# Optimization experiments

Measured on AMD Instinct MI355X. Metric: run time of the kernel, lower is better.

The kernel has to match this reference:

```python
import jax, jax.numpy as jnp
import numpy as np

SEQ_LEN, IN_DIM = 120, 132
UNITS = (64, 128, 64)
N_LABELS = 101


def _lstm(x, W, U, b):
    """Keras-style LSTM with activation='relu', recurrent_activation='sigmoid'.
    x: (B,T,D), W: (D,4u), U: (u,4u), b: (4u,). Gate order i,f,c,o.
    Returns full hidden sequence (B,T,u)."""
    u = U.shape[0]
    # precompute input projections for all timesteps (big GEMM outside scan)
    xz = jnp.einsum('btd,dz->btz', x, W) + b  # (B,T,4u)

    def step(carry, z_t):
        h, c = carry
        z = z_t + h @ U  # (B,4u)
        i, f, g, o = jnp.split(z, 4, axis=-1)
        i = jax.nn.sigmoid(i)
        f = jax.nn.sigmoid(f)
        o = jax.nn.sigmoid(o)
        c = f * c + i * jax.nn.relu(g)
        h = o * jax.nn.relu(c)
        return (h, c), h

    B = x.shape[0]
    h0 = jnp.zeros((B, u), x.dtype)
    (_, _), hs = jax.lax.scan(step, (h0, h0), jnp.swapaxes(xz, 0, 1))
    return jnp.swapaxes(hs, 0, 1)  # (B,T,u)


def setup_inputs() -> dict:
    key = jax.random.key(0)
    ks = jax.random.split(key, 16)
    s = 0.05
    d = {'x': jax.random.normal(ks[0], (1024, SEQ_LEN, IN_DIM), jnp.float32)}
    in_dims = (IN_DIM,) + UNITS[:-1]
    for l, (din, u) in enumerate(zip(in_dims, UNITS), start=1):
        d[f'W{l}'] = jax.random.normal(ks[3 * l - 2], (din, 4 * u), jnp.float32) * s
        d[f'U{l}'] = jax.random.normal(ks[3 * l - 1], (u, 4 * u), jnp.float32) * s
        d[f'b{l}'] = jnp.zeros((4 * u,), jnp.float32)
    dense_dims = [(UNITS[-1], 64), (64, 32), (32, N_LABELS)]
    for l, (din, dout) in enumerate(dense_dims, start=1):
        d[f'Wd{l}'] = jax.random.normal(ks[9 + l], (din, dout), jnp.float32) * s
        d[f'bd{l}'] = jnp.zeros((dout,), jnp.float32)
    return d


def reference(x, W1, U1, b1, W2, U2, b2, W3, U3, b3,
              Wd1, bd1, Wd2, bd2, Wd3, bd3):
    h = _lstm(x, W1, U1, b1)          # (B,T,64)
    h = _lstm(h, W2, U2, b2)          # (B,T,128)
    h = _lstm(h, W3, U3, b3)[:, -1]   # return_sequences=False -> (B,64)
    h = jax.nn.relu(h @ Wd1 + bd1)    # (B,64)
    h = jax.nn.relu(h @ Wd2 + bd2)    # (B,32)
    return jax.nn.softmax(h @ Wd3 + bd3, axis=-1)  # (B,101)
```

## Files before the change

### kernel.cpp

```cpp
#include <hip/hip_runtime.h>
#include <math.h>

#define T_STEPS 120
#define BATCH   1024
#define NBK     64

typedef __attribute__((ext_vector_type(8))) short bf16x8;
typedef __attribute__((ext_vector_type(4))) float f32x4;
typedef __attribute__((ext_vector_type(4))) unsigned short us4;
typedef unsigned short u16;

__device__ __forceinline__ unsigned split2(float f) {
    union { float f; unsigned u; } a; a.f = f;
    unsigned hi = a.u >> 16;
    union { float f; unsigned u; } h; h.u = a.u & 0xFFFF0000u;
    union { float f; unsigned u; } b; b.f = f - h.f;
    unsigned rr = b.u + 0x7FFFu + ((b.u >> 16) & 1);
    return (hi << 16) | (rr >> 16);
}

__device__ __forceinline__ short bf16rne(float f) {
    union { float f; unsigned u; } a; a.f = f;
    unsigned r = a.u + 0x7FFFu + ((a.u >> 16) & 1);
    return (short)(r >> 16);
}

__device__ __forceinline__ float fast_sigmoid(float x) {
    float e = __expf(-x);
    return __builtin_amdgcn_rcpf(1.f + e);
}

__device__ __forceinline__ void block_sync_lds() {
    asm volatile("s_waitcnt lgkmcnt(0)" ::: "memory");
    __builtin_amdgcn_sched_barrier(0);
    __builtin_amdgcn_s_barrier();
    __builtin_amdgcn_sched_barrier(0);
}

__global__ __launch_bounds__(256)
void xconv(const float* __restrict__ x, u16* __restrict__ xf)
{
    int tid  = blockIdx.x * 256 + threadIdx.x;
    int lane = tid & 63;
    int rest = tid >> 6;
    int kt   = rest % 5;
    int tbk  = rest / 5;
    int bk   = tbk & 63;
    int t    = tbk >> 6;
    int ln   = lane & 15, lq = lane >> 4;
    int b    = bk * 16 + ln;
    int k0   = kt * 32 + lq * 8;
    const float* src = &x[((size_t)b * T_STEPS + t) * 132];
    u16 out[8];
#pragma unroll
    for (int e = 0; e < 8; ++e) {
        int k = k0 + e;
        out[e] = (u16)bf16rne((k < 132) ? src[k] : 0.f);
    }
    us4 o0, o1;
    o0.x = out[0]; o0.y = out[1]; o0.z = out[2]; o0.w = out[3];
    o1.x = out[4]; o1.y = out[5]; o1.z = out[6]; o1.w = out[7];
    *reinterpret_cast<us4*>(&xf[(size_t)tid * 8])     = o0;
    *reinterpret_cast<us4*>(&xf[(size_t)tid * 8 + 4]) = o1;
}

template<int U, int NBT, int KTXI, int KTXO, bool LAST_ONLY>
__global__ __launch_bounds__(512, 1)
void lstm_comb(const u16* __restrict__ xf,
               const float* __restrict__ W, int KIN,
               const float* __restrict__ Uw, const float* __restrict__ bias,
               u16* __restrict__ hf, float* __restrict__ hlast)
{
    constexpr int NZ  = 4 * U;
    constexpr int KTH = U / 32;
    constexpr int KXP = KTXI * 32;
    constexpr int HPLANE = NBT * U;
    constexpr int UG  = U / 16;
    constexpr size_t XSTRIDE = (size_t)NBK * KTXI * 512;
    constexpr size_t OSTRIDE = (size_t)NBK * KTXO * 512;
    static_assert(UG * (NBT / 16) == 8, "8 waves");

    __shared__ u16 hsh[4 * HPLANE];
    __shared__ u16 Wl[KXP * NZ];

    const int tid  = threadIdx.x;
    const int lane = tid & 63;
    const int wid  = tid >> 6;
    const int ln   = lane & 15;
    const int lq   = lane >> 4;
    const int ug   = wid % UG;
    const int bh   = wid / UG;
    const int unit = ug * 16 + ln;
    const int bb   = bh * 16;
    const int b0   = blockIdx.x * NBT;
    const int bkw  = (b0 + bb) >> 4;

    for (int idx = tid; idx < KXP * NZ; idx += 512) {
        int k = idx / NZ, n = idx % NZ;
        float f = (k < KIN) ? W[(size_t)k * NZ + n] : 0.f;
        Wl[((k >> 3) * NZ + n) * 8 + (k & 7)] = (u16)bf16rne(f);
    }

    bf16x8 bwu[4][KTH];
#pragma unroll
    for (int p = 0; p < 4; ++p)
#pragma unroll
        for (int kt = 0; kt < KTH; ++kt)
#pragma unroll
            for (int e = 0; e < 8; ++e) {
                int k = kt * 32 + lq * 8 + e;
                bwu[p][kt][e] = bf16rne(Uw[(size_t)k * NZ + p * U + unit]);
            }
    float breg[4];
#pragma unroll
    for (int p = 0; p < 4; ++p) breg[p] = bias[p * U + unit];

    u16* hw0 = hsh + ((unit >> 3) * NBT + bb + lq * 4) * 8 + (unit & 7);
    u16* hw1 = hw0 + 2 * HPLANE;
    float creg[4];
#pragma unroll
    for (int r = 0; r < 4; ++r) {
        creg[r] = 0.f;
        hw0[r * 8] = 0;
        hw0[HPLANE + r * 8] = 0;
    }

    const u16* hrd[2][KTH];
#pragma unroll
    for (int b = 0; b < 2; ++b)
#pragma unroll
        for (int kt = 0; kt < KTH; ++kt)
            hrd[b][kt] = hsh + b * 2 * HPLANE + ((kt * 4 + lq) * NBT + bb + ln) * 8;

    const u16* wb = Wl + ((size_t)lq * NZ + unit) * 8;

    const u16* pxf = xf + ((size_t)bkw * KTXI) * 512 + lane * 8;
    bf16x8 xfh[KTXI];
#pragma unroll
    for (int kt = 0; kt < KTXI; ++kt)
        xfh[kt] = *reinterpret_cast<const bf16x8*>(pxf + kt * 512);

    u16* hfo = nullptr;
    if constexpr (!LAST_ONLY) {
        int kto = unit >> 5;
        int lqp = (unit >> 3) & 3;
        int ep  = unit & 7;
        hfo = hf + (((size_t)bkw * KTXO + kto) * 64 + lqp * 16 + lq * 4) * 8 + ep;
    }

    block_sync_lds();

#define CSTEP(CUR, OTH, tc)                                                     \
    {                                                                           \
        f32x4 acc[4] = {};                                                      \
        _Pragma("unroll")                                                       \
        for (int kt = 0; kt < KTH; ++kt) {                                      \
            bf16x8 ahh = *reinterpret_cast<const bf16x8*>(hrd[CUR][kt]);        \
            bf16x8 ahl = *reinterpret_cast<const bf16x8*>(hrd[CUR][kt] + HPLANE); \
            _Pragma("unroll")                                                   \
            for (int p = 0; p < 4; ++p) {                                       \
                acc[p] = __builtin_amdgcn_mfma_f32_16x16x32_bf16(ahh, bwu[p][kt], acc[p], 0, 0, 0); \
                acc[p] = __builtin_amdgcn_mfma_f32_16x16x32_bf16(ahl, bwu[p][kt], acc[p], 0, 0, 0); \
            }                                                                   \
        }                                                                       \
        _Pragma("unroll")                                                       \
        for (int kt = 0; kt < KTXI; ++kt)                                       \
        _Pragma("unroll")                                                       \
        for (int p = 0; p < 4; ++p) {                                           \
            bf16x8 wf = *reinterpret_cast<const bf16x8*>(wb + ((size_t)kt * 4 * NZ + p * U) * 8); \
            acc[p] = __builtin_amdgcn_mfma_f32_16x16x32_bf16(xfh[kt], wf, acc[p], 0, 0, 0); \
        }                                                                       \
        if ((tc) + 1 < T_STEPS) {                                               \
            pxf += XSTRIDE;                                                     \
            _Pragma("unroll")                                                   \
            for (int kt = 0; kt < KTXI; ++kt)                                   \
                xfh[kt] = *reinterpret_cast<const bf16x8*>(pxf + kt * 512);     \
        }                                                                       \
        _Pragma("unroll")                                                       \
        for (int r = 0; r < 4; ++r) {                                           \
            float si = fast_sigmoid(acc[0][r] + breg[0]);                       \
            float sf = fast_sigmoid(acc[1][r] + breg[1]);                       \
            float gg = fmaxf(acc[2][r] + breg[2], 0.f);                         \
            float so = fast_sigmoid(acc[3][r] + breg[3]);                       \
            float c  = sf * creg[r] + si * gg;                                  \
            creg[r] = c;                                                        \
            float h = so * fmaxf(c, 0.f);                                       \
            unsigned s = split2(h);                                             \
            u16* hw = (OTH) ? hw1 : hw0;                                        \
            hw[r * 8] = (u16)(s >> 16);                                         \
            hw[HPLANE + r * 8] = (u16)s;                                        \
            if constexpr (!LAST_ONLY) {                                         \
                hfo[(size_t)(tc) * OSTRIDE + r * 8] = (u16)(s >> 16);           \
            } else {                                                            \
                if ((tc) == T_STEPS - 1)                                        \
                    hlast[(size_t)(b0 + bb + lq * 4 + r) * U + unit] = h;       \
            }                                                                   \
        }                                                                       \
        block_sync_lds();                                                       \
    }

    for (int t = 0; t < T_STEPS; t += 2) {
        CSTEP(0, 1, t)
        CSTEP(1, 0, t + 1)
    }
#undef CSTEP
}

__global__ __launch_bounds__(256)
void dense_head(const float* __restrict__ h3,
                const float* __restrict__ Wd1, const float* __restrict__ bd1,
                const float* __restrict__ Wd2, const float* __restrict__ bd2,
                const float* __restrict__ Wd3, const float* __restrict__ bd3,
                float* __restrict__ out)
{
    __shared__ float s1[4][64];
    __shared__ float s2[4][32];
    const int w    = threadIdx.x >> 6;
    const int lane = threadIdx.x & 63;
    const int row  = blockIdx.x * 4 + w;

    float hval = h3[(size_t)row * 64 + lane];
    float a = bd1[lane];
#pragma unroll
    for (int k = 0; k < 64; ++k) {
        float hk = __shfl(hval, k, 64);
        a = fmaf(hk, Wd1[k * 64 + lane], a);
    }
    s1[w][lane] = fmaxf(a, 0.f);
    __syncthreads();

    if (lane < 32) {
        float a2 = bd2[lane];
#pragma unroll
        for (int k = 0; k < 64; ++k) a2 = fmaf(s1[w][k], Wd2[k * 32 + lane], a2);
        s2[w][lane] = fmaxf(a2, 0.f);
    }
    __syncthreads();

    float a0 = bd3[lane];
#pragma unroll
    for (int k = 0; k < 32; ++k) a0 = fmaf(s2[w][k], Wd3[k * 101 + lane], a0);
    float a1 = -INFINITY;
    if (lane < 37) {
        a1 = bd3[64 + lane];
#pragma unroll
        for (int k = 0; k < 32; ++k) a1 = fmaf(s2[w][k], Wd3[k * 101 + 64 + lane], a1);
    }

    float m = fmaxf(a0, a1);
#pragma unroll
    for (int off = 32; off > 0; off >>= 1) m = fmaxf(m, __shfl_xor(m, off, 64));
    float e0 = expf(a0 - m);
    float e1 = (lane < 37) ? expf(a1 - m) : 0.f;
    float s = e0 + e1;
#pragma unroll
    for (int off = 32; off > 0; off >>= 1) s += __shfl_xor(s, off, 64);

    out[(size_t)row * 101 + lane] = e0 / s;
    if (lane < 37) out[(size_t)row * 101 + 64 + lane] = e1 / s;
}

extern "C" void kernel_launch(void* const* d_in, const int* in_sizes, int n_in,
                              void* d_out, int out_size, void* d_ws, size_t ws_size,
                              hipStream_t stream) {
    const float* x   = (const float*)d_in[0];
    const float* W1  = (const float*)d_in[1];
    const float* U1  = (const float*)d_in[2];
    const float* b1  = (const float*)d_in[3];
    const float* W2  = (const float*)d_in[4];
    const float* U2  = (const float*)d_in[5];
    const float* b2  = (const float*)d_in[6];
    const float* W3  = (const float*)d_in[7];
    const float* U3  = (const float*)d_in[8];
    const float* b3  = (const float*)d_in[9];
    const float* Wd1 = (const float*)d_in[10];
    const float* bd1 = (const float*)d_in[11];
    const float* Wd2 = (const float*)d_in[12];
    const float* bd2 = (const float*)d_in[13];
    const float* Wd3 = (const float*)d_in[14];
    const float* bd3 = (const float*)d_in[15];

    u16* ws16 = (u16*)d_ws;
    u16* xfb  = ws16;
    u16* h1f  = ws16 + 19660800;
    u16* h2f  = h1f + 7864320;
    float* h3 = (float*)(ws16 + 43253760);

    xconv<<<(T_STEPS * NBK * 5 * 64) / 256, 256, 0, stream>>>(x, xfb);
    lstm_comb<64, 32, 5, 2, false><<<32, 512, 0, stream>>>(
        xfb, W1, 132, U1, b1, h1f, nullptr);
    lstm_comb<128, 16, 2, 4, false><<<64, 512, 0, stream>>>(
        h1f, W2, 64, U2, b2, h2f, nullptr);
    lstm_comb<64, 32, 4, 1, true><<<32, 512, 0, stream>>>(
        h2f, W3, 128, U3, b3, nullptr, h3);
    dense_head<<<BATCH / 4, 256, 0, stream>>>(h3, Wd1, bd1, Wd2, bd2, Wd3, bd3,
                                              (float*)d_out);
}
```

Measured before the change: 495.8 us.

## Halve LSTM waves per block, give each wave two tiles, drop split-bf16 hidden state

Each LSTM block now runs 4 waves instead of 8, and each wave computes two 16x16 tiles, either two unit groups or two batch halves. Layers 1 and 3 hold their input weights in registers rather than LDS. The recurrent hidden state is stored as a single bf16 instead of a hi/lo bf16 pair, which halves the recurrent MFMAs and the LDS traffic. This is meant to cut barrier cost and per-step latency on the serial recurrence. The trade-off is lower precision in the recurrent matmul and more work per wave.

After: 601.3 us. 1.21x slower.

```diff
diff --git a/kernel.cpp b/kernel.cpp
--- a/kernel.cpp
+++ b/kernel.cpp
@@ -9,15 +9,6 @@
 typedef __attribute__((ext_vector_type(4))) float f32x4;
 typedef __attribute__((ext_vector_type(4))) unsigned short us4;
 typedef unsigned short u16;
-
-__device__ __forceinline__ unsigned split2(float f) {
-    union { float f; unsigned u; } a; a.f = f;
-    unsigned hi = a.u >> 16;
-    union { float f; unsigned u; } h; h.u = a.u & 0xFFFF0000u;
-    union { float f; unsigned u; } b; b.f = f - h.f;
-    unsigned rr = b.u + 0x7FFFu + ((b.u >> 16) & 1);
-    return (hi << 16) | (rr >> 16);
-}
 
 __device__ __forceinline__ short bf16rne(float f) {
     union { float f; unsigned u; } a; a.f = f;
@@ -64,146 +55,210 @@
     *reinterpret_cast<us4*>(&xf[(size_t)tid * 8 + 4]) = o1;
 }
 
-template<int U, int NBT, int KTXI, int KTXO, bool LAST_ONLY>
-__global__ __launch_bounds__(512, 1)
-void lstm_comb(const u16* __restrict__ xf,
-               const float* __restrict__ W, int KIN,
-               const float* __restrict__ Uw, const float* __restrict__ bias,
-               u16* __restrict__ hf, float* __restrict__ hlast)
+template<int U, int NBT, int KTXI, int KTXO, bool UNITPH, bool WXLDS, bool LAST_ONLY>
+__global__ __launch_bounds__(256, 1)
+__attribute__((amdgpu_waves_per_eu(1, 1)))
+void lstm_ph(const u16* __restrict__ xf,
+             const float* __restrict__ W, int KIN,
+             const float* __restrict__ Uw, const float* __restrict__ bias,
+             u16* __restrict__ hf, float* __restrict__ hlast)
 {
     constexpr int NZ  = 4 * U;
     constexpr int KTH = U / 32;
-    constexpr int KXP = KTXI * 32;
     constexpr int HPLANE = NBT * U;
-    constexpr int UG  = U / 16;
+    constexpr int PHU = UNITPH ? 2 : 1;
+    constexpr int PHB = UNITPH ? 1 : 2;
     constexpr size_t XSTRIDE = (size_t)NBK * KTXI * 512;
     constexpr size_t OSTRIDE = (size_t)NBK * KTXO * 512;
-    static_assert(UG * (NBT / 16) == 8, "8 waves");
-
-    __shared__ u16 hsh[4 * HPLANE];
-    __shared__ u16 Wl[KXP * NZ];
+
+    __shared__ u16 hsh[2 * HPLANE];
+    __shared__ u16 Wl[WXLDS ? KTXI * 32 * NZ : 64];
 
     const int tid  = threadIdx.x;
     const int lane = tid & 63;
     const int wid  = tid >> 6;
     const int ln   = lane & 15;
     const int lq   = lane >> 4;
-    const int ug   = wid % UG;
-    const int bh   = wid / UG;
-    const int unit = ug * 16 + ln;
-    const int bb   = bh * 16;
     const int b0   = blockIdx.x * NBT;
-    const int bkw  = (b0 + bb) >> 4;
-
-    for (int idx = tid; idx < KXP * NZ; idx += 512) {
-        int k = idx / NZ, n = idx % NZ;
-        float f = (k < KIN) ? W[(size_t)k * NZ + n] : 0.f;
-        Wl[((k >> 3) * NZ + n) * 8 + (k & 7)] = (u16)bf16rne(f);
-    }
-
-    bf16x8 bwu[4][KTH];
-#pragma unroll
-    for (int p = 0; p < 4; ++p)
-#pragma unroll
-        for (int kt = 0; kt < KTH; ++kt)
-#pragma unroll
-            for (int e = 0; e < 8; ++e) {
-                int k = kt * 32 + lq * 8 + e;
-                bwu[p][kt][e] = bf16rne(Uw[(size_t)k * NZ + p * U + unit]);
-            }
-    float breg[4];
-#pragma unroll
-    for (int p = 0; p < 4; ++p) breg[p] = bias[p * U + unit];
-
-    u16* hw0 = hsh + ((unit >> 3) * NBT + bb + lq * 4) * 8 + (unit & 7);
-    u16* hw1 = hw0 + 2 * HPLANE;
-    float creg[4];
-#pragma unroll
-    for (int r = 0; r < 4; ++r) {
-        creg[r] = 0.f;
-        hw0[r * 8] = 0;
-        hw0[HPLANE + r * 8] = 0;
-    }
-
-    const u16* hrd[2][KTH];
-#pragma unroll
-    for (int b = 0; b < 2; ++b)
-#pragma unroll
-        for (int kt = 0; kt < KTH; ++kt)
-            hrd[b][kt] = hsh + b * 2 * HPLANE + ((kt * 4 + lq) * NBT + bb + ln) * 8;
-
-    const u16* wb = Wl + ((size_t)lq * NZ + unit) * 8;
-
-    const u16* pxf = xf + ((size_t)bkw * KTXI) * 512 + lane * 8;
-    bf16x8 xfh[KTXI];
-#pragma unroll
-    for (int kt = 0; kt < KTXI; ++kt)
-        xfh[kt] = *reinterpret_cast<const bf16x8*>(pxf + kt * 512);
-
-    u16* hfo = nullptr;
+
+    int unitp[2], bbp[2];
+#pragma unroll
+    for (int pp = 0; pp < 2; ++pp) {
+        unitp[pp] = (UNITPH ? (wid + 4 * pp) : wid) * 16 + ln;
+        bbp[pp]   = UNITPH ? 0 : pp * 16;
+    }
+
+    if constexpr (WXLDS) {
+        for (int idx = tid; idx < KTXI * 32 * NZ; idx += 256) {
+            int k = idx / NZ, n = idx % NZ;
+            float f = (k < KIN) ? W[(size_t)k * NZ + n] : 0.f;
+            Wl[((k >> 3) * NZ + n) * 8 + (k & 7)] = (u16)bf16rne(f);
+        }
+    }
+
+    bf16x8 bwu[PHU][4][KTH];
+#pragma unroll
+    for (int up = 0; up < PHU; ++up)
+#pragma unroll
+        for (int p4 = 0; p4 < 4; ++p4)
+#pragma unroll
+            for (int kt = 0; kt < KTH; ++kt)
+#pragma unroll
+                for (int e = 0; e < 8; ++e) {
+                    int k = kt * 32 + lq * 8 + e;
+                    bwu[up][p4][kt][e] = bf16rne(Uw[(size_t)k * NZ + p4 * U + unitp[up]]);
+                }
+    float breg[PHU][4];
+#pragma unroll
+    for (int up = 0; up < PHU; ++up)
+#pragma unroll
+        for (int p4 = 0; p4 < 4; ++p4) breg[up][p4] = bias[p4 * U + unitp[up]];
+
+    bf16x8 wxw[4][KTXI];
+    if constexpr (!WXLDS) {
+#pragma unroll
+        for (int p4 = 0; p4 < 4; ++p4)
+#pragma unroll
+            for (int kt = 0; kt < KTXI; ++kt)
+#pragma unroll
+                for (int e = 0; e < 8; ++e) {
+                    int k = kt * 32 + lq * 8 + e;
+                    wxw[p4][kt][e] = (k < KIN) ? bf16rne(W[(size_t)k * NZ + p4 * U + unitp[0]])
+                                               : (short)0;
+                }
+    }
+
+    const u16* wbp[2];
+#pragma unroll
+    for (int pp = 0; pp < 2; ++pp)
+        wbp[pp] = Wl + ((size_t)lq * NZ + unitp[pp]) * 8;
+
+    u16* hwp[2][2];
+    float creg[2][4];
+#pragma unroll
+    for (int pp = 0; pp < 2; ++pp) {
+        int base = ((unitp[pp] >> 3) * NBT + bbp[pp] + lq * 4) * 8 + (unitp[pp] & 7);
+        hwp[pp][0] = hsh + base;
+        hwp[pp][1] = hsh + HPLANE + base;
+#pragma unroll
+        for (int r = 0; r < 4; ++r) {
+            creg[pp][r] = 0.f;
+            hwp[pp][0][r * 8] = 0;
+        }
+    }
+
+    const u16* hrd[2][PHB][KTH];
+#pragma unroll
+    for (int bf = 0; bf < 2; ++bf)
+#pragma unroll
+        for (int pb = 0; pb < PHB; ++pb)
+#pragma unroll
+            for (int kt = 0; kt < KTH; ++kt)
+                hrd[bf][pb][kt] = hsh + bf * HPLANE + ((kt * 4 + lq) * NBT + bbp[pb] + ln) * 8;
+
+    const u16* pxf[PHB];
+    bf16x8 xfh[PHB][KTXI];
+#pragma unroll
+    for (int pb = 0; pb < PHB; ++pb) {
+        int bkw = (b0 + bbp[pb]) >> 4;
+        pxf[pb] = xf + (size_t)bkw * KTXI * 512 + lane * 8;
+#pragma unroll
+        for (int kt = 0; kt < KTXI; ++kt)
+            xfh[pb][kt] = *reinterpret_cast<const bf16x8*>(pxf[pb] + kt * 512);
+    }
+
+    u16* hfo[2] = {nullptr, nullptr};
     if constexpr (!LAST_ONLY) {
-        int kto = unit >> 5;
-        int lqp = (unit >> 3) & 3;
-        int ep  = unit & 7;
-        hfo = hf + (((size_t)bkw * KTXO + kto) * 64 + lqp * 16 + lq * 4) * 8 + ep;
+#pragma unroll
+        for (int pp = 0; pp < 2; ++pp) {
+            int kto = unitp[pp] >> 5;
+            int lqp = (unitp[pp] >> 3) & 3;
+            int ep  = unitp[pp] & 7;
+            int bkw = (b0 + bbp[pp]) >> 4;
+            hfo[pp] = hf + (((size_t)bkw * KTXO + kto) * 64 + lqp * 16 + lq * 4) * 8 + ep;
+        }
     }
 
     block_sync_lds();
 
-#define CSTEP(CUR, OTH, tc)                                                     \
+#define PSTEP(CUR, OTH, tc)                                                     \
     {                                                                           \
-        f32x4 acc[4] = {};                                                      \
-        _Pragma("unroll")                                                       \
-        for (int kt = 0; kt < KTH; ++kt) {                                      \
-            bf16x8 ahh = *reinterpret_cast<const bf16x8*>(hrd[CUR][kt]);        \
-            bf16x8 ahl = *reinterpret_cast<const bf16x8*>(hrd[CUR][kt] + HPLANE); \
+        bf16x8 ah[PHB][KTH];                                                    \
+        _Pragma("unroll")                                                       \
+        for (int pb = 0; pb < PHB; ++pb)                                        \
+        _Pragma("unroll")                                                       \
+        for (int kt = 0; kt < KTH; ++kt)                                        \
+            ah[pb][kt] = *reinterpret_cast<const bf16x8*>(hrd[CUR][pb][kt]);    \
+        f32x4 acc[2][4] = {};                                                   \
+                                  \
+        _Pragma("unroll")                                                       \
+        for (int pp = 0; pp < 2; ++pp) {                                        \
+            constexpr int _dummy = 0; (void)_dummy;                             \
             _Pragma("unroll")                                                   \
-            for (int p = 0; p < 4; ++p) {                                       \
-                acc[p] = __builtin_amdgcn_mfma_f32_16x16x32_bf16(ahh, bwu[p][kt], acc[p], 0, 0, 0); \
-                acc[p] = __builtin_amdgcn_mfma_f32_16x16x32_bf16(ahl, bwu[p][kt], acc[p], 0, 0, 0); \
+            for (int kt = 0; kt < KTXI; ++kt)                                   \
+            _Pragma("unroll")                                                   \
+            for (int p4 = 0; p4 < 4; ++p4) {                                    \
+                bf16x8 wf;                                                      \
+                if constexpr (WXLDS)                                            \
+                    wf = *reinterpret_cast<const bf16x8*>(                      \
+                        wbp[pp] + ((size_t)kt * 4 * NZ + p4 * U) * 8);          \
+                else                                                            \
+                    wf = wxw[p4][kt];                                           \
+                acc[pp][p4] = __builtin_amdgcn_mfma_f32_16x16x32_bf16(          \
+                    xfh[UNITPH ? 0 : pp][kt], wf, acc[pp][p4], 0, 0, 0);        \
             }                                                                   \
         }                                                                       \
-        _Pragma("unroll")                                                       \
-        for (int kt = 0; kt < KTXI; ++kt)                                       \
-        _Pragma("unroll")                                                       \
-        for (int p = 0; p < 4; ++p) {                                           \
-            bf16x8 wf = *reinterpret_cast<const bf16x8*>(wb + ((size_t)kt * 4 * NZ + p * U) * 8); \
-            acc[p] = __builtin_amdgcn_mfma_f32_16x16x32_bf16(xfh[kt], wf, acc[p], 0, 0, 0); \
+                                                                    \
+        _Pragma("unroll")                                                       \
+        for (int pp = 0; pp < 2; ++pp)                                          \
+        _Pragma("unroll")                                                       \
+        for (int kt = 0; kt < KTH; ++kt)                                        \
+        _Pragma("unroll")                                                       \
+        for (int p4 = 0; p4 < 4; ++p4)                                          \
+            acc[pp][p4] = __builtin_amdgcn_mfma_f32_16x16x32_bf16(              \
+                ah[UNITPH ? 0 : pp][kt], bwu[UNITPH ? pp : 0][p4][kt],          \
+                acc[pp][p4], 0, 0, 0);                                          \
+                                                           \
+        if ((tc) + 1 < T_STEPS) {                                               \
+            _Pragma("unroll")                                                   \
+            for (int pb = 0; pb < PHB; ++pb) {                                  \
+                pxf[pb] += XSTRIDE;                                             \
+                _Pragma("unroll")                                               \
+                for (int kt = 0; kt < KTXI; ++kt)                               \
+                    xfh[pb][kt] = *reinterpret_cast<const bf16x8*>(pxf[pb] + kt * 512); \
+            }                                                                   \
         }                                                                       \
-        if ((tc) + 1 < T_STEPS) {                                               \
-            pxf += XSTRIDE;                                                     \
+                                                  \
+        _Pragma("unroll")                                                       \
+        for (int pp = 0; pp < 2; ++pp) {                                        \
+            const int up = UNITPH ? pp : 0;                                     \
             _Pragma("unroll")                                                   \
-            for (int kt = 0; kt < KTXI; ++kt)                                   \
-                xfh[kt] = *reinterpret_cast<const bf16x8*>(pxf + kt * 512);     \
-        }                                                                       \
-        _Pragma("unroll")                                                       \
-        for (int r = 0; r < 4; ++r) {                                           \
-            float si = fast_sigmoid(acc[0][r] + breg[0]);                       \
-            float sf = fast_sigmoid(acc[1][r] + breg[1]);                       \
-            float gg = fmaxf(acc[2][r] + breg[2], 0.f);                         \
-            float so = fast_sigmoid(acc[3][r] + breg[3]);                       \
-            float c  = sf * creg[r] + si * gg;                                  \
-            creg[r] = c;                                                        \
-            float h = so * fmaxf(c, 0.f);                                       \
-            unsigned s = split2(h);                                             \
-            u16* hw = (OTH) ? hw1 : hw0;                                        \
-            hw[r * 8] = (u16)(s >> 16);                                         \
-            hw[HPLANE + r * 8] = (u16)s;                                        \
-            if constexpr (!LAST_ONLY) {                                         \
-                hfo[(size_t)(tc) * OSTRIDE + r * 8] = (u16)(s >> 16);           \
-            } else {                                                            \
-                if ((tc) == T_STEPS - 1)                                        \
-                    hlast[(size_t)(b0 + bb + lq * 4 + r) * U + unit] = h;       \
+            for (int r = 0; r < 4; ++r) {                                       \
+                float si = fast_sigmoid(acc[pp][0][r] + breg[up][0]);           \
+                float sf = fast_sigmoid(acc[pp][1][r] + breg[up][1]);           \
+                float gg = fmaxf(acc[pp][2][r] + breg[up][2], 0.f);             \
+                float so = fast_sigmoid(acc[pp][3][r] + breg[up][3]);           \
+                float c  = sf * creg[pp][r] + si * gg;                          \
+                creg[pp][r] = c;                                                \
+                float h = so * fmaxf(c, 0.f);                                   \
+                u16 hb = (u16)bf16rne(h);                                       \
+                hwp[pp][OTH][r * 8] = hb;                                       \
+                if constexpr (!LAST_ONLY) {                                     \
+                    hfo[pp][(size_t)(tc) * OSTRIDE + r * 8] = hb;               \
+                } else {                                                        \
+                    if ((tc) == T_STEPS - 1)                                    \
+                        hlast[(size_t)(b0 + bbp[pp] + lq * 4 + r) * U + unitp[pp]] = h; \
+                }                                                               \
             }                                                                   \
         }                                                                       \
         block_sync_lds();                                                       \
     }
 
     for (int t = 0; t < T_STEPS; t += 2) {
-        CSTEP(0, 1, t)
-        CSTEP(1, 0, t + 1)
-    }
-#undef CSTEP
+        PSTEP(0, 1, t)
+        PSTEP(1, 0, t + 1)
+    }
+#undef PSTEP
 }
 
 __global__ __launch_bounds__(256)
@@ -287,11 +342,11 @@
     float* h3 = (float*)(ws16 + 43253760);
 
     xconv<<<(T_STEPS * NBK * 5 * 64) / 256, 256, 0, stream>>>(x, xfb);
-    lstm_comb<64, 32, 5, 2, false><<<32, 512, 0, stream>>>(
+    lstm_ph<64, 32, 5, 2, false, false, false><<<32, 256, 0, stream>>>(
         xfb, W1, 132, U1, b1, h1f, nullptr);
-    lstm_comb<128, 16, 2, 4, false><<<64, 512, 0, stream>>>(
+    lstm_ph<128, 16, 2, 4, true, true, false><<<64, 256, 0, stream>>>(
         h1f, W2, 64, U2, b2, h2f, nullptr);
-    lstm_comb<64, 32, 4, 1, true><<<32, 512, 0, stream>>>(
+    lstm_ph<64, 32, 4, 1, false, false, true><<<32, 256, 0, stream>>>(
         h2f, W3, 128, U3, b3, nullptr, h3);
     dense_head<<<BATCH / 4, 256, 0, stream>>>(h3, Wd1, bd1, Wd2, bd2, Wd3, bd3,
                                               (float*)d_out);
```
